# Performance work log

Measured on AMD Instinct MI355X. Metric: run time of the kernel, lower is better.

## Reference

```python
import jax, jax.numpy as jnp
import numpy as np

B, S, D = 4, 1024, 1024
H, DK = 16, 64

def setup_inputs() -> dict:
    key = jax.random.key(0)
    ks = jax.random.split(key, 12)
    s = lambda k, shape, scale: (jax.random.normal(k, shape, dtype=jnp.float32) * scale)
    inp = {
        "query": s(ks[0], (B, S, D), 1.0),
        "key":   s(ks[1], (B, S, D), 1.0),
        "value": s(ks[2], (B, S, D), 1.0),
        # per-head query projections stacked: [H, D, DK]
        "Wq": s(ks[3], (H, D, DK), D ** -0.5),
        "bq": jnp.zeros((H, DK), jnp.float32),
        # shared key / value projections (MQA)
        "Wk": s(ks[4], (D, DK), D ** -0.5),
        "bk": jnp.zeros((DK,), jnp.float32),
        "Wv": s(ks[5], (D, DK), D ** -0.5),
        "bv": jnp.zeros((DK,), jnp.float32),
        # combine_heads: Dense(key_dim) applied to concat of H head outputs
        "Wc": s(ks[6], (H * DK, DK), (H * DK) ** -0.5),
        "bc": jnp.zeros((DK,), jnp.float32),
    }
    return inp


def reference(query, key, value, Wq, bq, Wk, bk, Wv, bv, Wc, bc):
    # per-head query projections, batched over heads: [B,H,S,DK]
    q = jnp.einsum('bsd,hdk->bhsk', query, Wq) + bq[None, :, None, :]
    # shared K/V (multi-query attention): [B,S,DK]
    k = jnp.einsum('bsd,dk->bsk', key, Wk) + bk
    v = jnp.einsum('bsd,dk->bsk', value, Wv) + bv
    scale = 1.0 / jnp.sqrt(jnp.asarray(DK, q.dtype))
    # scores: [B,H,S,S], K broadcast across heads
    scores = jnp.einsum('bhsk,btk->bhst', q, k) * scale
    attn = jax.nn.softmax(scores, axis=-1)
    # head outputs: [B,H,S,DK]
    out_h = jnp.einsum('bhst,btk->bhsk', attn, v)
    # concat heads along last axis (head order preserved): [B,S,H*DK]
    concat = out_h.transpose(0, 2, 1, 3).reshape(B, S, H * DK)
    output = concat @ Wc + bc  # [B,S,DK]; dropout=0.0 -> identity
    return output, attn
```

## Files before the change

### kernel.cpp

```cpp
#include <hip/hip_runtime.h>

typedef __bf16 bf16;
typedef __attribute__((ext_vector_type(4))) float f32x4;
typedef __attribute__((ext_vector_type(8))) bf16 bf16x8;
typedef __attribute__((ext_vector_type(4))) bf16 bf16x4;

constexpr int Bc = 4, Sc = 1024, Dc = 1024, Hc = 16, DKc = 64;


__device__ __forceinline__ void stage64(bf16* s, const void* g, int ld, int f32src) {
  const int t = threadIdx.x;
#pragma unroll
  for (int i = 0; i < 2; ++i) {
    const int G = t + i * 256;
    const int r = G >> 3, gr = G & 7;
    bf16x8 o;
    if (f32src) {
      const float* gp = (const float*)g + (long)r * ld + gr * 8;
      const f32x4 a = *(const f32x4*)gp;
      const f32x4 b = *(const f32x4*)(gp + 4);
      o[0]=(bf16)a[0]; o[1]=(bf16)a[1]; o[2]=(bf16)a[2]; o[3]=(bf16)a[3];
      o[4]=(bf16)b[0]; o[5]=(bf16)b[1]; o[6]=(bf16)b[2]; o[7]=(bf16)b[3];
    } else {
      o = *(const bf16x8*)((const bf16*)g + (long)r * ld + gr * 8);
    }
    *(bf16x8*)(s + r * 64 + ((gr * 8) ^ ((r & 7) << 3))) = o;
  }
}

__device__ __forceinline__ bf16x8 frag_ld(const bf16* s, int row, int kofs) {
  const int lane = threadIdx.x & 63;
  const int c0 = kofs + (((lane >> 4) & 3) << 2);
  const int sw = (row & 7) << 3;
  union { bf16x8 v8; bf16x4 v4[2]; } u;
  u.v4[0] = *(const bf16x4*)(s + row * 64 + (c0 ^ sw));
  u.v4[1] = *(const bf16x4*)(s + row * 64 + ((c0 + 16) ^ sw));
  return u.v8;
}

__device__ __forceinline__ void gld16(const bf16* g, bf16* l) {
  __builtin_amdgcn_global_load_lds(
      (const __attribute__((address_space(1))) void*)g,
      (__attribute__((address_space(3))) void*)l, 16, 0, 0);
}

#define WAIT_BAR(vm) do { \
  asm volatile("s_waitcnt vmcnt(" vm ")" ::: "memory"); \
  __builtin_amdgcn_s_barrier(); \
  __builtin_amdgcn_sched_barrier(0); } while (0)

__global__ __launch_bounds__(256) void transpose_weights(
    const float* __restrict__ Wq, const float* __restrict__ Wk,
    const float* __restrict__ Wv, const float* __restrict__ Wc,
    bf16* __restrict__ WqT, bf16* __restrict__ WkT,
    bf16* __restrict__ WvT, bf16* __restrict__ WcT) {
  const int bid = blockIdx.x;
  const float* src; bf16* dst; float scl; int r0;
  if (bid < 256)      { const int hh = bid >> 4; r0 = (bid & 15) * 64;
                        src = Wq + (hh << 16); dst = WqT + (hh << 16); scl = 0.125f; }
  else if (bid < 272) { r0 = (bid - 256) * 64; src = Wk; dst = WkT; scl = 1.f; }
  else if (bid < 288) { r0 = (bid - 272) * 64; src = Wv; dst = WvT; scl = 1.f; }
  else                { r0 = (bid - 288) * 64; src = Wc; dst = WcT; scl = 1.f; }

  __shared__ float tile[64][68];
  const int t = threadIdx.x;
  const int rr = t >> 4, cc = (t & 15) * 4;
#pragma unroll
  for (int i = 0; i < 4; ++i) {
    const f32x4 v = *(const f32x4*)(src + (long)(r0 + rr + i * 16) * 64 + cc);
    *(f32x4*)(&tile[rr + i * 16][cc]) = v;
  }
  __syncthreads();
#pragma unroll
  for (int i = 0; i < 2; ++i) {
    const int g = t + i * 256, orow = g >> 3, oc = (g & 7) * 8;
    bf16x8 o;
#pragma unroll
    for (int jj = 0; jj < 8; ++jj) o[jj] = (bf16)(tile[oc + jj][orow] * scl);
    *(bf16x8*)(dst + (long)orow * 1024 + r0 + oc) = o;
  }
}

__global__ __launch_bounds__(256) void proj_kernel(
    const float* __restrict__ query, const float* __restrict__ key,
    const float* __restrict__ value, const bf16* __restrict__ WqT,
    const bf16* __restrict__ WkT, const bf16* __restrict__ WvT,
    const float* __restrict__ bq, const float* __restrict__ bk,
    const float* __restrict__ bv, bf16* __restrict__ q_cat,
    bf16* __restrict__ k_proj, bf16* __restrict__ vTp) {
  const int bid = blockIdx.x;
  const void* A; const void* BT; bf16* C; const float* bias;
  int m0, n0, ldA, ldBT, ldC, aF32, bF32, biasM;
  float bscale;
  if (bid < 1024) {
    m0 = (bid >> 4) << 6; n0 = (bid & 15) << 6;
    A = query; ldA = 1024; aF32 = 1;
    BT = WqT;  ldBT = 1024; bF32 = 0;
    C = q_cat; ldC = 1024; bias = bq; biasM = 0; bscale = 0.125f;
  } else if (bid < 1088) {
    m0 = (bid - 1024) << 6; n0 = 0;
    A = key;    ldA = 1024; aF32 = 1;
    BT = WkT;   ldBT = 1024; bF32 = 0;
    C = k_proj; ldC = 64; bias = bk; biasM = 0; bscale = 1.f;
  } else {
    const int j = bid - 1088;
    m0 = 0; n0 = (j & 15) << 6;
    A = WvT; ldA = 1024; aF32 = 0;
    BT = value + ((long)(j >> 4) << 20); ldBT = 1024; bF32 = 1;
    C = vTp + ((long)(j >> 4) << 16); ldC = 1024; bias = bv; biasM = 1; bscale = 1.f;
  }

  __shared__ bf16 sA[2][4096];
  __shared__ bf16 sB[2][4096];
  const int lane = threadIdx.x & 63;
  const int w = threadIdx.x >> 6;

  f32x4 acc[4];
#pragma unroll
  for (int nb = 0; nb < 4; ++nb) acc[nb] = (f32x4){0.f, 0.f, 0.f, 0.f};

  stage64(sA[0], aF32 ? (const void*)((const float*)A + (long)m0 * ldA)
                      : (const void*)((const bf16*)A + (long)m0 * ldA), ldA, aF32);
  stage64(sB[0], bF32 ? (const void*)((const float*)BT + (long)n0 * ldBT)
                      : (const void*)((const bf16*)BT + (long)n0 * ldBT), ldBT, bF32);
  __syncthreads();

  for (int it = 0; it < 16; ++it) {
    const int p = it & 1;
    if (it < 15) {
      const int kk = (it + 1) * 64;
      stage64(sA[p ^ 1], aF32 ? (const void*)((const float*)A + (long)m0 * ldA + kk)
                              : (const void*)((const bf16*)A + (long)m0 * ldA + kk), ldA, aF32);
      stage64(sB[p ^ 1], bF32 ? (const void*)((const float*)BT + (long)n0 * ldBT + kk)
                              : (const void*)((const bf16*)BT + (long)n0 * ldBT + kk), ldBT, bF32);
    }
#pragma unroll
    for (int ks = 0; ks < 2; ++ks) {
      const bf16x8 af = frag_ld(sA[p], 16 * w + (lane & 15), ks * 32);
#pragma unroll
      for (int nb = 0; nb < 4; ++nb) {
        const bf16x8 bfr = frag_ld(sB[p], nb * 16 + (lane & 15), ks * 32);
        acc[nb] = __builtin_amdgcn_mfma_f32_16x16x32_bf16(af, bfr, acc[nb], 0, 0, 0);
      }
    }
    __syncthreads();
  }

  const int rbase = m0 + 16 * w + ((lane >> 4) << 2);
#pragma unroll
  for (int nb = 0; nb < 4; ++nb) {
    const int col = n0 + nb * 16 + (lane & 15);
    const float bn = biasM ? 0.f : bias[col] * bscale;
#pragma unroll
    for (int r = 0; r < 4; ++r) {
      const int row = rbase + r;
      C[(long)row * ldC + col] = (bf16)(acc[nb][r] + (biasM ? bias[row] : bn));
    }
  }
}

__global__ __launch_bounds__(256) void combine_kernel(
    const bf16* __restrict__ concat, const bf16* __restrict__ WcT,
    float* __restrict__ part) {
  const int ks = blockIdx.x >> 6;
  const int m0 = (blockIdx.x & 63) * 64;
  const int k0 = ks * 256;
  __shared__ bf16 sA[2][4096];
  __shared__ bf16 sB[2][4096];
  const int lane = threadIdx.x & 63;
  const int w = threadIdx.x >> 6;

  f32x4 acc[4];
#pragma unroll
  for (int nb = 0; nb < 4; ++nb) acc[nb] = (f32x4){0.f, 0.f, 0.f, 0.f};

  stage64(sA[0], concat + (long)m0 * 1024 + k0, 1024, 0);
  stage64(sB[0], WcT + k0, 1024, 0);
  __syncthreads();
  for (int it = 0; it < 4; ++it) {
    const int p = it & 1;
    if (it < 3) {
      const int kk = k0 + (it + 1) * 64;
      stage64(sA[p ^ 1], concat + (long)m0 * 1024 + kk, 1024, 0);
      stage64(sB[p ^ 1], WcT + kk, 1024, 0);
    }
#pragma unroll
    for (int ksl = 0; ksl < 2; ++ksl) {
      const bf16x8 af = frag_ld(sA[p], 16 * w + (lane & 15), ksl * 32);
#pragma unroll
      for (int nb = 0; nb < 4; ++nb) {
        const bf16x8 bfr = frag_ld(sB[p], nb * 16 + (lane & 15), ksl * 32);
        acc[nb] = __builtin_amdgcn_mfma_f32_16x16x32_bf16(af, bfr, acc[nb], 0, 0, 0);
      }
    }
    __syncthreads();
  }
  const int rbase = m0 + 16 * w + ((lane >> 4) << 2);
  float* pb = part + (long)ks * 262144;
#pragma unroll
  for (int nb = 0; nb < 4; ++nb) {
    const int col = nb * 16 + (lane & 15);
#pragma unroll
    for (int r = 0; r < 4; ++r)
      pb[(long)(rbase + r) * 64 + col] = acc[nb][r];
  }
}

__global__ __launch_bounds__(256) void reduce_combine(
    const float* __restrict__ part, const float* __restrict__ bc,
    float* __restrict__ out0) {
  const int i = blockIdx.x * 256 + threadIdx.x;
  out0[i] = part[i] + part[i + 262144] + part[i + 524288] + part[i + 786432]
          + bc[i & 63];
}

__global__ __launch_bounds__(128, 4) void attn_kernel(
    const bf16* __restrict__ q_cat, const bf16* __restrict__ k_proj,
    const bf16* __restrict__ vT, float* __restrict__ attn_out,
    bf16* __restrict__ concat) {
  const int s0 = blockIdx.x * 64;
  const int h = blockIdx.y, b = blockIdx.z;
  const int t = threadIdx.x;
  const int lane = t & 63;
  const int w = t >> 6;

  __shared__ bf16 sK[2][4096];
  __shared__ bf16 sV[2][4096];

  const bf16* kp = k_proj + (long)b * Sc * DKc;
  const bf16* vp = vT + (long)b * DKc * Sc;
  float* ao = attn_out + ((long)(b * Hc + h) * Sc + s0) * Sc;
  bf16* co = concat + (long)(b * Sc + s0) * (Hc * DKc) + h * DKc;

  const int c0q = (lane >> 4) << 2;
  const int wq0 = w * 32;

  const int rloc = t >> 3;
  const int col8 = ((t & 7) ^ (rloc & 7)) << 3;
  const int ldsw = w << 9;

  auto stageK = [&](int pb, int tt) {
#pragma unroll
    for (int c = 0; c < 4; ++c)
      gld16(kp + ((long)tt << 12) + (c * 16 + rloc) * 64 + col8,
            &sK[pb][c * 1024 + ldsw]);
  };
  auto stageV = [&](int pb, int tt) {
#pragma unroll
    for (int c = 0; c < 4; ++c)
      gld16(vp + (long)(c * 16 + rloc) * 1024 + tt * 64 + col8,
            &sV[pb][c * 1024 + ldsw]);
  };

  bf16x8 qf[2][2];
#pragma unroll
  for (int qg = 0; qg < 2; ++qg) {
    const bf16* qrow = q_cat + (long)(b * Sc + s0 + wq0 + qg * 16 + (lane & 15)) * 1024 + h * 64;
    union { bf16x8 v8; bf16x4 v4[2]; } a, c;
    a.v4[0] = *(const bf16x4*)(qrow + c0q);
    a.v4[1] = *(const bf16x4*)(qrow + c0q + 16);
    c.v4[0] = *(const bf16x4*)(qrow + c0q + 32);
    c.v4[1] = *(const bf16x4*)(qrow + c0q + 48);
    qf[qg][0] = a.v8; qf[qg][1] = c.v8;
  }

  stageK(0, 0);
  WAIT_BAR("0");
  float lsum[2] = {0.f, 0.f};
  for (int tc = 0; tc < 16; ++tc) {
    const int p = tc & 1;
    if (tc < 15) stageK(p ^ 1, tc + 1);
    bf16x8 kf[2][4];
#pragma unroll
    for (int ks = 0; ks < 2; ++ks)
#pragma unroll
      for (int nb = 0; nb < 4; ++nb)
        kf[ks][nb] = frag_ld(sK[p], nb * 16 + (lane & 15), ks * 32);
#pragma unroll
    for (int qg = 0; qg < 2; ++qg) {
      f32x4 sc[4];
#pragma unroll
      for (int nb = 0; nb < 4; ++nb) sc[nb] = (f32x4){0.f, 0.f, 0.f, 0.f};
#pragma unroll
      for (int ks = 0; ks < 2; ++ks)
#pragma unroll
        for (int nb = 0; nb < 4; ++nb)
          sc[nb] = __builtin_amdgcn_mfma_f32_16x16x32_bf16(kf[ks][nb], qf[qg][ks], sc[nb], 0, 0, 0);
#pragma unroll
      for (int nb = 0; nb < 4; ++nb)
#pragma unroll
        for (int r = 0; r < 4; ++r) lsum[qg] += __expf(sc[nb][r]);
    }
    if (tc < 15) WAIT_BAR("0");
  }

#pragma unroll
  for (int qg = 0; qg < 2; ++qg) {
    lsum[qg] += __shfl_xor(lsum[qg], 16, 64);
    lsum[qg] += __shfl_xor(lsum[qg], 32, 64);
  }
  const float invl0 = 1.f / lsum[0], invl1 = 1.f / lsum[1];

  f32x4 oacc[2][4];
#pragma unroll
  for (int qg = 0; qg < 2; ++qg)
#pragma unroll
    for (int nb = 0; nb < 4; ++nb) oacc[qg][nb] = (f32x4){0.f, 0.f, 0.f, 0.f};

  stageK(0, 0);
  stageV(0, 0);
  WAIT_BAR("0");
  for (int tc = 0; tc < 16; ++tc) {
    const int p = tc & 1;
    if (tc < 15) { stageK(p ^ 1, tc + 1); stageV(p ^ 1, tc + 1); }
    bf16x8 kf[2][4];
#pragma unroll
    for (int ks = 0; ks < 2; ++ks)
#pragma unroll
      for (int nb = 0; nb < 4; ++nb)
        kf[ks][nb] = frag_ld(sK[p], nb * 16 + (lane & 15), ks * 32);
    bf16x8 pa[2][2];
#pragma unroll
    for (int qg = 0; qg < 2; ++qg) {
      f32x4 sc[4];
#pragma unroll
      for (int nb = 0; nb < 4; ++nb) sc[nb] = (f32x4){0.f, 0.f, 0.f, 0.f};
#pragma unroll
      for (int ks = 0; ks < 2; ++ks)
#pragma unroll
        for (int nb = 0; nb < 4; ++nb)
          sc[nb] = __builtin_amdgcn_mfma_f32_16x16x32_bf16(kf[ks][nb], qf[qg][ks], sc[nb], 0, 0, 0);
      const float invl = qg ? invl1 : invl0;
      float* aobase = ao + (long)(wq0 + qg * 16 + (lane & 15)) * Sc + tc * 64 + c0q;
      float e[4][4];
#pragma unroll
      for (int nb = 0; nb < 4; ++nb) {
#pragma unroll
        for (int r = 0; r < 4; ++r) e[nb][r] = __expf(sc[nb][r]);
        f32x4 av;
#pragma unroll
        for (int r = 0; r < 4; ++r) av[r] = e[nb][r] * invl;
        *(f32x4*)(aobase + nb * 16) = av;
      }
#pragma unroll
      for (int ks = 0; ks < 2; ++ks)
#pragma unroll
        for (int jj = 0; jj < 4; ++jj) {
          pa[qg][ks][jj]     = (bf16)e[2 * ks][jj];
          pa[qg][ks][4 + jj] = (bf16)e[2 * ks + 1][jj];
        }
    }
#pragma unroll
    for (int ks = 0; ks < 2; ++ks)
#pragma unroll
      for (int nb = 0; nb < 4; ++nb) {
        const bf16x8 vf = frag_ld(sV[p], nb * 16 + (lane & 15), ks * 32);
        oacc[0][nb] = __builtin_amdgcn_mfma_f32_16x16x32_bf16(pa[0][ks], vf, oacc[0][nb], 0, 0, 0);
        oacc[1][nb] = __builtin_amdgcn_mfma_f32_16x16x32_bf16(pa[1][ks], vf, oacc[1][nb], 0, 0, 0);
      }
    if (tc < 15) WAIT_BAR("8");
  }

#pragma unroll
  for (int qg = 0; qg < 2; ++qg) {
    const float invl = qg ? invl1 : invl0;
    float invo[4];
#pragma unroll
    for (int r = 0; r < 4; ++r) invo[r] = __shfl(invl, c0q + r, 64);
#pragma unroll
    for (int nb = 0; nb < 4; ++nb) {
#pragma unroll
      for (int r = 0; r < 4; ++r) {
        const int row = wq0 + qg * 16 + c0q + r;
        const int col = nb * 16 + (lane & 15);
        co[(long)row * (Hc * DKc) + col] = (bf16)(oacc[qg][nb][r] * invo[r]);
      }
    }
  }
}


extern "C" void kernel_launch(void* const* d_in, const int* in_sizes, int n_in,
                              void* d_out, int out_size, void* d_ws, size_t ws_size,
                              hipStream_t stream) {
  const float* query = (const float*)d_in[0];
  const float* key   = (const float*)d_in[1];
  const float* value = (const float*)d_in[2];
  const float* Wq = (const float*)d_in[3];
  const float* bq = (const float*)d_in[4];
  const float* Wk = (const float*)d_in[5];
  const float* bk = (const float*)d_in[6];
  const float* Wv = (const float*)d_in[7];
  const float* bv = (const float*)d_in[8];
  const float* Wc = (const float*)d_in[9];
  const float* bc = (const float*)d_in[10];

  bf16* WqT    = (bf16*)d_ws;
  bf16* WkT    = WqT + 1048576;
  bf16* WvT    = WkT + 65536;
  bf16* WcT    = WvT + 65536;
  bf16* q_cat  = WcT + 65536;
  bf16* k_proj = q_cat + 4194304;
  bf16* vTp    = k_proj + 262144;
  bf16* concat = vTp + 262144;
  float* part  = (float*)(concat + 4194304);

  float* out0 = (float*)d_out;
  float* attn = out0 + (long)Bc * Sc * DKc;

  transpose_weights<<<304, 256, 0, stream>>>(Wq, Wk, Wv, Wc, WqT, WkT, WvT, WcT);

  proj_kernel<<<1152, 256, 0, stream>>>(query, key, value, WqT, WkT, WvT,
                                        bq, bk, bv, q_cat, k_proj, vTp);

  attn_kernel<<<dim3(16, 16, 4), 128, 0, stream>>>(q_cat, k_proj, vTp, attn, concat);

  combine_kernel<<<256, 256, 0, stream>>>(concat, WcT, part);
  reduce_combine<<<1024, 256, 0, stream>>>(part, bc, out0);
}
```

Measured before the change: 186.7 us.

## Split attention into PV/rowsum pass and separate probability-write pass using exp2

Folds log2(e)/sqrt(dk) into the Q projection scale so softmax uses the hardware exp2 directly. The attention kernel is split in two. The core pass computes the row sums and P·V in one sweep, then stores the inverse row sums. A second kernel recomputes QK^T and writes the normalised 256MB probability matrix. This removes the separate row-sum pre-pass from the PV kernel and decouples the large attention-matrix store from the MMA-heavy kernel, at the cost of an extra kernel launch and a recomputation of the scores. Unnormalised exponentials without a max subtraction are kept, so overflow risk is the same as before.

```diff
diff --git a/kernel.cpp b/kernel.cpp
--- a/kernel.cpp
+++ b/kernel.cpp
@@ -6,6 +6,8 @@
 typedef __attribute__((ext_vector_type(4))) bf16 bf16x4;
 
 constexpr int Bc = 4, Sc = 1024, Dc = 1024, Hc = 16, DKc = 64;
+#define ESCALE 0.18033688011112042f
+#define EXP2F(x) __builtin_amdgcn_exp2f(x)
 
 
 __device__ __forceinline__ void stage64(bf16* s, const void* g, int ld, int f32src) {
@@ -57,7 +59,7 @@
   const int bid = blockIdx.x;
   const float* src; bf16* dst; float scl; int r0;
   if (bid < 256)      { const int hh = bid >> 4; r0 = (bid & 15) * 64;
-                        src = Wq + (hh << 16); dst = WqT + (hh << 16); scl = 0.125f; }
+                        src = Wq + (hh << 16); dst = WqT + (hh << 16); scl = ESCALE; }
   else if (bid < 272) { r0 = (bid - 256) * 64; src = Wk; dst = WkT; scl = 1.f; }
   else if (bid < 288) { r0 = (bid - 272) * 64; src = Wv; dst = WvT; scl = 1.f; }
   else                { r0 = (bid - 288) * 64; src = Wc; dst = WcT; scl = 1.f; }
@@ -96,7 +98,7 @@
     m0 = (bid >> 4) << 6; n0 = (bid & 15) << 6;
     A = query; ldA = 1024; aF32 = 1;
     BT = WqT;  ldBT = 1024; bF32 = 0;
-    C = q_cat; ldC = 1024; bias = bq; biasM = 0; bscale = 0.125f;
+    C = q_cat; ldC = 1024; bias = bq; biasM = 0; bscale = ESCALE;
   } else if (bid < 1088) {
     m0 = (bid - 1024) << 6; n0 = 0;
     A = key;    ldA = 1024; aF32 = 1;
@@ -214,9 +216,9 @@
           + bc[i & 63];
 }
 
-__global__ __launch_bounds__(128, 4) void attn_kernel(
+__global__ __launch_bounds__(128) void attn_core(
     const bf16* __restrict__ q_cat, const bf16* __restrict__ k_proj,
-    const bf16* __restrict__ vT, float* __restrict__ attn_out,
+    const bf16* __restrict__ vT, float* __restrict__ lsinv,
     bf16* __restrict__ concat) {
   const int s0 = blockIdx.x * 64;
   const int h = blockIdx.y, b = blockIdx.z;
@@ -229,8 +231,8 @@
 
   const bf16* kp = k_proj + (long)b * Sc * DKc;
   const bf16* vp = vT + (long)b * DKc * Sc;
-  float* ao = attn_out + ((long)(b * Hc + h) * Sc + s0) * Sc;
   bf16* co = concat + (long)(b * Sc + s0) * (Hc * DKc) + h * DKc;
+  float* li = lsinv + ((long)(b * Hc + h) * Sc + s0);
 
   const int c0q = (lane >> 4) << 2;
   const int wq0 = w * 32;
@@ -264,43 +266,7 @@
     qf[qg][0] = a.v8; qf[qg][1] = c.v8;
   }
 
-  stageK(0, 0);
-  WAIT_BAR("0");
   float lsum[2] = {0.f, 0.f};
-  for (int tc = 0; tc < 16; ++tc) {
-    const int p = tc & 1;
-    if (tc < 15) stageK(p ^ 1, tc + 1);
-    bf16x8 kf[2][4];
-#pragma unroll
-    for (int ks = 0; ks < 2; ++ks)
-#pragma unroll
-      for (int nb = 0; nb < 4; ++nb)
-        kf[ks][nb] = frag_ld(sK[p], nb * 16 + (lane & 15), ks * 32);
-#pragma unroll
-    for (int qg = 0; qg < 2; ++qg) {
-      f32x4 sc[4];
-#pragma unroll
-      for (int nb = 0; nb < 4; ++nb) sc[nb] = (f32x4){0.f, 0.f, 0.f, 0.f};
-#pragma unroll
-      for (int ks = 0; ks < 2; ++ks)
-#pragma unroll
-        for (int nb = 0; nb < 4; ++nb)
-          sc[nb] = __builtin_amdgcn_mfma_f32_16x16x32_bf16(kf[ks][nb], qf[qg][ks], sc[nb], 0, 0, 0);
-#pragma unroll
-      for (int nb = 0; nb < 4; ++nb)
-#pragma unroll
-        for (int r = 0; r < 4; ++r) lsum[qg] += __expf(sc[nb][r]);
-    }
-    if (tc < 15) WAIT_BAR("0");
-  }
-
-#pragma unroll
-  for (int qg = 0; qg < 2; ++qg) {
-    lsum[qg] += __shfl_xor(lsum[qg], 16, 64);
-    lsum[qg] += __shfl_xor(lsum[qg], 32, 64);
-  }
-  const float invl0 = 1.f / lsum[0], invl1 = 1.f / lsum[1];
-
   f32x4 oacc[2][4];
 #pragma unroll
   for (int qg = 0; qg < 2; ++qg)
@@ -330,18 +296,14 @@
 #pragma unroll
         for (int nb = 0; nb < 4; ++nb)
           sc[nb] = __builtin_amdgcn_mfma_f32_16x16x32_bf16(kf[ks][nb], qf[qg][ks], sc[nb], 0, 0, 0);
-      const float invl = qg ? invl1 : invl0;
-      float* aobase = ao + (long)(wq0 + qg * 16 + (lane & 15)) * Sc + tc * 64 + c0q;
       float e[4][4];
 #pragma unroll
-      for (int nb = 0; nb < 4; ++nb) {
-#pragma unroll
-        for (int r = 0; r < 4; ++r) e[nb][r] = __expf(sc[nb][r]);
-        f32x4 av;
-#pragma unroll
-        for (int r = 0; r < 4; ++r) av[r] = e[nb][r] * invl;
-        *(f32x4*)(aobase + nb * 16) = av;
-      }
+      for (int nb = 0; nb < 4; ++nb)
+#pragma unroll
+        for (int r = 0; r < 4; ++r) {
+          e[nb][r] = EXP2F(sc[nb][r]);
+          lsum[qg] += e[nb][r];
+        }
 #pragma unroll
       for (int ks = 0; ks < 2; ++ks)
 #pragma unroll
@@ -358,7 +320,18 @@
         oacc[0][nb] = __builtin_amdgcn_mfma_f32_16x16x32_bf16(pa[0][ks], vf, oacc[0][nb], 0, 0, 0);
         oacc[1][nb] = __builtin_amdgcn_mfma_f32_16x16x32_bf16(pa[1][ks], vf, oacc[1][nb], 0, 0, 0);
       }
-    if (tc < 15) WAIT_BAR("8");
+    if (tc < 15) WAIT_BAR("0");
+  }
+
+#pragma unroll
+  for (int qg = 0; qg < 2; ++qg) {
+    lsum[qg] += __shfl_xor(lsum[qg], 16, 64);
+    lsum[qg] += __shfl_xor(lsum[qg], 32, 64);
+  }
+  const float invl0 = 1.f / lsum[0], invl1 = 1.f / lsum[1];
+  if (lane < 16) {
+    li[wq0 + lane] = invl0;
+    li[wq0 + 16 + lane] = invl1;
   }
 
 #pragma unroll
@@ -376,6 +349,81 @@
         co[(long)row * (Hc * DKc) + col] = (bf16)(oacc[qg][nb][r] * invo[r]);
       }
     }
+  }
+}
+
+__global__ __launch_bounds__(256) void attn_write(
+    const bf16* __restrict__ q_cat, const bf16* __restrict__ k_proj,
+    const float* __restrict__ lsinv, float* __restrict__ attn_out) {
+  const int s0 = blockIdx.x * 128;
+  const int h = blockIdx.y, b = blockIdx.z;
+  const int t = threadIdx.x;
+  const int lane = t & 63;
+  const int w = t >> 6;
+
+  __shared__ bf16 sK[2][4096];
+
+  const bf16* kp = k_proj + (long)b * Sc * DKc;
+  float* ao = attn_out + ((long)(b * Hc + h) * Sc + s0) * Sc;
+  const float* li = lsinv + ((long)(b * Hc + h) * Sc + s0);
+
+  const int c0q = (lane >> 4) << 2;
+  const int wq0 = w * 32;
+
+  const int col8 = ((lane & 7) ^ (lane >> 3)) << 3;
+  auto stageK = [&](int pb, int tt) {
+#pragma unroll
+    for (int i = 0; i < 2; ++i)
+      gld16(kp + ((long)tt << 12) + (w * 16 + i * 8 + (lane >> 3)) * 64 + col8,
+            &sK[pb][w * 1024 + i * 512]);
+  };
+
+  bf16x8 qf[2][2];
+  float linv[2];
+#pragma unroll
+  for (int qg = 0; qg < 2; ++qg) {
+    const int row = wq0 + qg * 16 + (lane & 15);
+    const bf16* qrow = q_cat + (long)(b * Sc + s0 + row) * 1024 + h * 64;
+    union { bf16x8 v8; bf16x4 v4[2]; } a, c;
+    a.v4[0] = *(const bf16x4*)(qrow + c0q);
+    a.v4[1] = *(const bf16x4*)(qrow + c0q + 16);
+    c.v4[0] = *(const bf16x4*)(qrow + c0q + 32);
+    c.v4[1] = *(const bf16x4*)(qrow + c0q + 48);
+    qf[qg][0] = a.v8; qf[qg][1] = c.v8;
+    linv[qg] = li[row];
+  }
+
+  stageK(0, 0);
+  WAIT_BAR("0");
+  for (int tc = 0; tc < 16; ++tc) {
+    const int p = tc & 1;
+    if (tc < 15) stageK(p ^ 1, tc + 1);
+    bf16x8 kf[2][4];
+#pragma unroll
+    for (int ks = 0; ks < 2; ++ks)
+#pragma unroll
+      for (int nb = 0; nb < 4; ++nb)
+        kf[ks][nb] = frag_ld(sK[p], nb * 16 + (lane & 15), ks * 32);
+#pragma unroll
+    for (int qg = 0; qg < 2; ++qg) {
+      f32x4 sc[4];
+#pragma unroll
+      for (int nb = 0; nb < 4; ++nb) sc[nb] = (f32x4){0.f, 0.f, 0.f, 0.f};
+#pragma unroll
+      for (int ks = 0; ks < 2; ++ks)
+#pragma unroll
+        for (int nb = 0; nb < 4; ++nb)
+          sc[nb] = __builtin_amdgcn_mfma_f32_16x16x32_bf16(kf[ks][nb], qf[qg][ks], sc[nb], 0, 0, 0);
+      float* aobase = ao + (long)(wq0 + qg * 16 + (lane & 15)) * Sc + tc * 64 + c0q;
+#pragma unroll
+      for (int nb = 0; nb < 4; ++nb) {
+        f32x4 av;
+#pragma unroll
+        for (int r = 0; r < 4; ++r) av[r] = EXP2F(sc[nb][r]) * linv[qg];
+        *(f32x4*)(aobase + nb * 16) = av;
+      }
+    }
+    if (tc < 15) WAIT_BAR("8");
   }
 }
 
@@ -404,6 +452,7 @@
   bf16* vTp    = k_proj + 262144;
   bf16* concat = vTp + 262144;
   float* part  = (float*)(concat + 4194304);
+  float* lsinv = part + 1048576;
 
   float* out0 = (float*)d_out;
   float* attn = out0 + (long)Bc * Sc * DKc;
@@ -413,7 +462,8 @@
   proj_kernel<<<1152, 256, 0, stream>>>(query, key, value, WqT, WkT, WvT,
                                         bq, bk, bv, q_cat, k_proj, vTp);
 
-  attn_kernel<<<dim3(16, 16, 4), 128, 0, stream>>>(q_cat, k_proj, vTp, attn, concat);
+  attn_core<<<dim3(16, 16, 4), 128, 0, stream>>>(q_cat, k_proj, vTp, lsinv, concat);
+  attn_write<<<dim3(8, 16, 4), 256, 0, stream>>>(q_cat, k_proj, lsinv, attn);
 
   combine_kernel<<<256, 256, 0, stream>>>(concat, WcT, part);
   reduce_combine<<<1024, 256, 0, stream>>>(part, bc, out0);
```

Result: slower. 203.3 us (+8.9%).

## Use 128x128 tiles for Q projection and fold log2e into scale for exp2

Applied to the files above, without the earlier changes.

The Q projection GEMM moves from 64x64 tiles to 128x128 tiles, with each wave computing a 4x4 grid of MFMA blocks and LDS rows XOR-swizzled. This raises operand reuse and cuts redundant fp32 query loads. The softmax scale now includes log2(e), so the attention kernel can call the hardware exp2 directly instead of __expf. The larger tiles mean fewer blocks, 256 instead of 1024, and more registers and LDS per block, which could lower occupancy.

```diff
diff --git a/kernel.cpp b/kernel.cpp
--- a/kernel.cpp
+++ b/kernel.cpp
@@ -6,6 +6,8 @@
 typedef __attribute__((ext_vector_type(4))) bf16 bf16x4;
 
 constexpr int Bc = 4, Sc = 1024, Dc = 1024, Hc = 16, DKc = 64;
+#define ESCALE 0.18033688011112042f
+#define EXP2F(x) __builtin_amdgcn_exp2f(x)
 
 
 __device__ __forceinline__ void stage64(bf16* s, const void* g, int ld, int f32src) {
@@ -57,7 +59,7 @@
   const int bid = blockIdx.x;
   const float* src; bf16* dst; float scl; int r0;
   if (bid < 256)      { const int hh = bid >> 4; r0 = (bid & 15) * 64;
-                        src = Wq + (hh << 16); dst = WqT + (hh << 16); scl = 0.125f; }
+                        src = Wq + (hh << 16); dst = WqT + (hh << 16); scl = ESCALE; }
   else if (bid < 272) { r0 = (bid - 256) * 64; src = Wk; dst = WkT; scl = 1.f; }
   else if (bid < 288) { r0 = (bid - 272) * 64; src = Wv; dst = WvT; scl = 1.f; }
   else                { r0 = (bid - 288) * 64; src = Wc; dst = WcT; scl = 1.f; }
@@ -88,32 +90,96 @@
     const float* __restrict__ bq, const float* __restrict__ bk,
     const float* __restrict__ bv, bf16* __restrict__ q_cat,
     bf16* __restrict__ k_proj, bf16* __restrict__ vTp) {
+  __shared__ bf16 sA[2][8192];
+  __shared__ bf16 sB[2][8192];
   const int bid = blockIdx.x;
+  const int t = threadIdx.x;
+  const int lane = t & 63;
+  const int w = t >> 6;
+
+  if (bid < 256) {
+    const int m0 = (bid >> 3) << 7, n0 = (bid & 7) << 7;
+    const int wr = w >> 1, wc = w & 1;
+
+    f32x4 acc[4][4];
+#pragma unroll
+    for (int mi = 0; mi < 4; ++mi)
+#pragma unroll
+      for (int ni = 0; ni < 4; ++ni) acc[mi][ni] = (f32x4){0.f, 0.f, 0.f, 0.f};
+
+    auto sQA = [&](int p, int kk) {
+      const int r = t >> 1, ch = (t & 1) << 5;
+      const float* gp = query + (long)(m0 + r) * 1024 + kk + ch;
+#pragma unroll
+      for (int j = 0; j < 4; ++j) {
+        const f32x4 a = *(const f32x4*)(gp + j * 8);
+        const f32x4 b = *(const f32x4*)(gp + j * 8 + 4);
+        bf16x8 o;
+        o[0]=(bf16)a[0]; o[1]=(bf16)a[1]; o[2]=(bf16)a[2]; o[3]=(bf16)a[3];
+        o[4]=(bf16)b[0]; o[5]=(bf16)b[1]; o[6]=(bf16)b[2]; o[7]=(bf16)b[3];
+        *(bf16x8*)(&sA[p][r * 64 + ((ch + j * 8) ^ ((r & 7) << 3))]) = o;
+      }
+    };
+    auto sQB = [&](int p, int kk) {
+#pragma unroll
+      for (int i = 0; i < 4; ++i) {
+        const int G = t + i * 256, r = G >> 3, c8 = (G & 7) << 3;
+        const bf16x8 v = *(const bf16x8*)(WqT + (long)(n0 + r) * 1024 + kk + c8);
+        *(bf16x8*)(&sB[p][r * 64 + (c8 ^ ((r & 7) << 3))]) = v;
+      }
+    };
+
+    sQA(0, 0); sQB(0, 0);
+    __syncthreads();
+    for (int it = 0; it < 16; ++it) {
+      const int p = it & 1;
+      if (it < 15) { sQA(p ^ 1, (it + 1) * 64); sQB(p ^ 1, (it + 1) * 64); }
+#pragma unroll
+      for (int ks = 0; ks < 2; ++ks) {
+        bf16x8 af[4], bfr[4];
+#pragma unroll
+        for (int mi = 0; mi < 4; ++mi)
+          af[mi] = frag_ld(sA[p], wr * 64 + mi * 16 + (lane & 15), ks * 32);
+#pragma unroll
+        for (int ni = 0; ni < 4; ++ni)
+          bfr[ni] = frag_ld(sB[p], wc * 64 + ni * 16 + (lane & 15), ks * 32);
+#pragma unroll
+        for (int mi = 0; mi < 4; ++mi)
+#pragma unroll
+          for (int ni = 0; ni < 4; ++ni)
+            acc[mi][ni] = __builtin_amdgcn_mfma_f32_16x16x32_bf16(af[mi], bfr[ni], acc[mi][ni], 0, 0, 0);
+      }
+      __syncthreads();
+    }
+
+    const int rb = m0 + wr * 64 + ((lane >> 4) << 2);
+#pragma unroll
+    for (int ni = 0; ni < 4; ++ni) {
+      const int col = n0 + wc * 64 + ni * 16 + (lane & 15);
+      const float bn = bq[col] * ESCALE;
+#pragma unroll
+      for (int mi = 0; mi < 4; ++mi)
+#pragma unroll
+        for (int r4 = 0; r4 < 4; ++r4)
+          q_cat[(long)(rb + mi * 16 + r4) * 1024 + col] = (bf16)(acc[mi][ni][r4] + bn);
+    }
+    return;
+  }
+
   const void* A; const void* BT; bf16* C; const float* bias;
   int m0, n0, ldA, ldBT, ldC, aF32, bF32, biasM;
-  float bscale;
-  if (bid < 1024) {
-    m0 = (bid >> 4) << 6; n0 = (bid & 15) << 6;
-    A = query; ldA = 1024; aF32 = 1;
-    BT = WqT;  ldBT = 1024; bF32 = 0;
-    C = q_cat; ldC = 1024; bias = bq; biasM = 0; bscale = 0.125f;
-  } else if (bid < 1088) {
-    m0 = (bid - 1024) << 6; n0 = 0;
+  if (bid < 320) {
+    m0 = (bid - 256) << 6; n0 = 0;
     A = key;    ldA = 1024; aF32 = 1;
     BT = WkT;   ldBT = 1024; bF32 = 0;
-    C = k_proj; ldC = 64; bias = bk; biasM = 0; bscale = 1.f;
+    C = k_proj; ldC = 64; bias = bk; biasM = 0;
   } else {
-    const int j = bid - 1088;
+    const int j = bid - 320;
     m0 = 0; n0 = (j & 15) << 6;
     A = WvT; ldA = 1024; aF32 = 0;
     BT = value + ((long)(j >> 4) << 20); ldBT = 1024; bF32 = 1;
-    C = vTp + ((long)(j >> 4) << 16); ldC = 1024; bias = bv; biasM = 1; bscale = 1.f;
-  }
-
-  __shared__ bf16 sA[2][4096];
-  __shared__ bf16 sB[2][4096];
-  const int lane = threadIdx.x & 63;
-  const int w = threadIdx.x >> 6;
+    C = vTp + ((long)(j >> 4) << 16); ldC = 1024; bias = bv; biasM = 1;
+  }
 
   f32x4 acc[4];
 #pragma unroll
@@ -150,7 +216,7 @@
 #pragma unroll
   for (int nb = 0; nb < 4; ++nb) {
     const int col = n0 + nb * 16 + (lane & 15);
-    const float bn = biasM ? 0.f : bias[col] * bscale;
+    const float bn = biasM ? 0.f : bias[col];
 #pragma unroll
     for (int r = 0; r < 4; ++r) {
       const int row = rbase + r;
@@ -289,7 +355,7 @@
 #pragma unroll
       for (int nb = 0; nb < 4; ++nb)
 #pragma unroll
-        for (int r = 0; r < 4; ++r) lsum[qg] += __expf(sc[nb][r]);
+        for (int r = 0; r < 4; ++r) lsum[qg] += EXP2F(sc[nb][r]);
     }
     if (tc < 15) WAIT_BAR("0");
   }
@@ -336,7 +402,7 @@
 #pragma unroll
       for (int nb = 0; nb < 4; ++nb) {
 #pragma unroll
-        for (int r = 0; r < 4; ++r) e[nb][r] = __expf(sc[nb][r]);
+        for (int r = 0; r < 4; ++r) e[nb][r] = EXP2F(sc[nb][r]);
         f32x4 av;
 #pragma unroll
         for (int r = 0; r < 4; ++r) av[r] = e[nb][r] * invl;
@@ -410,8 +476,8 @@
 
   transpose_weights<<<304, 256, 0, stream>>>(Wq, Wk, Wv, Wc, WqT, WkT, WvT, WcT);
 
-  proj_kernel<<<1152, 256, 0, stream>>>(query, key, value, WqT, WkT, WvT,
-                                        bq, bk, bv, q_cat, k_proj, vTp);
+  proj_kernel<<<384, 256, 0, stream>>>(query, key, value, WqT, WkT, WvT,
+                                       bq, bk, bv, q_cat, k_proj, vTp);
 
   attn_kernel<<<dim3(16, 16, 4), 128, 0, stream>>>(q_cat, k_proj, vTp, attn, concat);
 
```

After: 160.3 us. 1.16x faster.
